# Kernel optimization log

Hardware: AMD Instinct MI355X
Metric: run time of the kernel (lower is better)

The kernel has to match this reference:

```python
import jax, jax.numpy as jnp
import numpy as np

IN_DIM = 256      # in_dim
OUT_DIM = 4608    # out_dim = 6*768 (adaLN projection)
M = 68            # ceil(sqrt(max(in_dim, out_dim)))
PAD = M * M       # 4624 padded (perfect-square) dim
B = 16384         # token batch
INIT_SCALE = 0.02


def setup_inputs() -> dict:
    key = jax.random.key(0)
    k1, k2, k3 = jax.random.split(key, 3)
    x = jax.random.normal(k1, (B, IN_DIM), dtype=jnp.float32)
    # Monarch block-diagonal factors: M blocks of M x M each, scaled per init_scale
    L = jax.random.normal(k2, (M, M, M), dtype=jnp.float32) * INIT_SCALE
    R = jax.random.normal(k3, (M, M, M), dtype=jnp.float32) * INIT_SCALE
    bias = jnp.zeros((OUT_DIM,), dtype=jnp.float32)
    return {"x": x, "L": L, "R": R, "bias": bias}


def _monarch_linear(x, L, R, bias):
    # zero-pad input up to the perfect-square dim n = M*M
    b = x.shape[0]
    xp = jnp.pad(x, ((0, 0), (0, PAD - IN_DIM)))          # [B, PAD]
    x2 = xp.reshape(b, M, M)                               # [B, k=M, p=M]
    # first block-diagonal matmul: per-block x @ L[k]^T
    t1 = jnp.einsum('bkp,kqp->bkq', x2, L)                 # [B, k, q]
    # Monarch inner permutation (block transpose)
    t1 = jnp.swapaxes(t1, 1, 2)                            # [B, l=q, r=k]
    # second block-diagonal matmul
    t2 = jnp.einsum('blr,lsr->bls', t1, R)                 # [B, l, s]
    y = jnp.swapaxes(t2, 1, 2).reshape(b, PAD)             # [B, PAD] (s-major)
    # slice to out_dim, add bias
    return y[:, :OUT_DIM] + bias


def reference(x, L, R, bias):
    return _monarch_linear(x, L, R, bias)
```

## Files before the change

kernel.cpp:

```cpp
#include <hip/hip_runtime.h>


typedef float f4 __attribute__((ext_vector_type(4)));

namespace {
constexpr int MM    = 68;
constexpr int IN_D  = 256;
constexpr int OUT_D = 4608;
constexpr int TT    = 16;
constexpr int NTH   = 256;
constexpr int NJ    = 5;
constexpr int XROW  = IN_D + 4;
constexpr int TPAD  = 4 * MM + 4;
}

template <int P4M>
__device__ __forceinline__ void phaseA(const float* __restrict__ xls,
                                       const float* __restrict__ Lrow0,
                                       float* __restrict__ t1w)
{
  float acc[17];
#pragma unroll
  for (int li = 0; li < 17; ++li) acc[li] = 0.f;

#pragma unroll 1
  for (int p4 = 0; p4 < P4M; ++p4) {
    f4 xv = *(const f4*)(xls + 4 * p4);
    f4 Lv[17];
#pragma unroll
    for (int li = 0; li < 17; ++li)
      Lv[li] = *(const f4*)(Lrow0 + (size_t)li * MM + 4 * p4);
#pragma unroll
    for (int li = 0; li < 17; ++li) {
      acc[li] = fmaf(xv.x, Lv[li].x, acc[li]);
      acc[li] = fmaf(xv.y, Lv[li].y, acc[li]);
      acc[li] = fmaf(xv.z, Lv[li].z, acc[li]);
      acc[li] = fmaf(xv.w, Lv[li].w, acc[li]);
    }
  }
#pragma unroll
  for (int li = 0; li < 17; ++li) t1w[li] = acc[li];
}

__global__ __launch_bounds__(NTH, 4)
void monarch_fused(const float* __restrict__ x, const float* __restrict__ L,
                   const float* __restrict__ R, const float* __restrict__ bias,
                   float* __restrict__ out)
{
  __shared__ float xs[TT * XROW];
  __shared__ float t1s[TT * TPAD];
  const int tid = threadIdx.x;
  const long tb = (long)blockIdx.x * TT;

#pragma unroll
  for (int k = 0; k < (TT * IN_D / 4) / NTH; ++k) {
    int i   = k * NTH + tid;
    int tok = i >> 6;
    int pos = i & 63;
    *(f4*)(&xs[tok * XROW + 4 * pos]) = *(const f4*)(x + (tb + tok) * IN_D + 4 * pos);
  }
  __syncthreads();

  {
    const int tok = tid & 15;
    const int seg = tid >> 4;
    const int r   = seg >> 2;
    const int lq  = seg & 3;
    const float* xls   = &xs[tok * XROW + r * MM];
    const float* Lrow0 = L + (size_t)(r * MM + lq * 17) * MM;
    float*       t1w   = &t1s[tok * TPAD + r * MM + lq * 17];
    if (r < 3) phaseA<17>(xls, Lrow0, t1w);
    else       phaseA<13>(xls, Lrow0, t1w);
  }
  __syncthreads();

  {
    const int g  = tid / 17;
    const int m  = tid - g * 17;
    const int l4 = 4 * m;

#pragma unroll 1
    for (int j = 0; j < NJ; ++j) {
      const int s = g + 15 * j;
      const bool act = (tid < 255) && (s < MM) && (s < MM - 1 || m < 13);
      const int scol = s * MM + l4;
      f4 R0, R1, R2, R3, bv;
      if (act) {
        R0 = *(const f4*)(R + (size_t)(l4 + 0) * (MM * MM) + (size_t)s * MM);
        R1 = *(const f4*)(R + (size_t)(l4 + 1) * (MM * MM) + (size_t)s * MM);
        R2 = *(const f4*)(R + (size_t)(l4 + 2) * (MM * MM) + (size_t)s * MM);
        R3 = *(const f4*)(R + (size_t)(l4 + 3) * (MM * MM) + (size_t)s * MM);
        bv = *(const f4*)(bias + scol);
      }
#pragma unroll 2
      for (int t = 0; t < TT; ++t) {
        if (act) {
          const float* t1p = t1s + t * TPAD + l4;
          f4 a0 = *(const f4*)(t1p);
          f4 a1 = *(const f4*)(t1p + MM);
          f4 a2 = *(const f4*)(t1p + 2 * MM);
          f4 a3 = *(const f4*)(t1p + 3 * MM);
          f4 o;
          o.x = fmaf(a3.x, R0.w, fmaf(a2.x, R0.z, fmaf(a1.x, R0.y, fmaf(a0.x, R0.x, bv.x))));
          o.y = fmaf(a3.y, R1.w, fmaf(a2.y, R1.z, fmaf(a1.y, R1.y, fmaf(a0.y, R1.x, bv.y))));
          o.z = fmaf(a3.z, R2.w, fmaf(a2.z, R2.z, fmaf(a1.z, R2.y, fmaf(a0.z, R2.x, bv.z))));
          o.w = fmaf(a3.w, R3.w, fmaf(a2.w, R3.z, fmaf(a1.w, R3.y, fmaf(a0.w, R3.x, bv.w))));
          *(f4*)(out + (tb + t) * OUT_D + scol) = o;
        }
      }
    }
  }
}

extern "C" void kernel_launch(void* const* d_in, const int* in_sizes, int n_in,
                              void* d_out, int out_size, void* d_ws, size_t ws_size,
                              hipStream_t stream) {
  const float* x    = (const float*)d_in[0];
  const float* L    = (const float*)d_in[1];
  const float* R    = (const float*)d_in[2];
  const float* bias = (const float*)d_in[3];
  float* out = (float*)d_out;

  const int ntok = in_sizes[0] / IN_D;
  monarch_fused<<<ntok / TT, NTH, 0, stream>>>(x, L, R, bias, out);
}
```

Baseline: 91.34 us.

## Interleave first-stage chunks with second-stage output writes inside each block

Phase A now runs in chunks of 4 tokens, with the threads split across token, block and row-quarter. Each chunk's first-stage products are computed while the second stage writes outputs for the previous chunk, with a barrier between chunks. The aim is to overlap the L-side compute with the large output store stream instead of running them as two separate phases. In exchange, R and bias are reloaded once per chunk, there are extra __syncthreads barriers, and the per-thread dot products are shorter.

```diff
diff --git a/kernel.cpp b/kernel.cpp
--- a/kernel.cpp
+++ b/kernel.cpp
@@ -8,30 +8,31 @@
 constexpr int IN_D  = 256;
 constexpr int OUT_D = 4608;
 constexpr int TT    = 16;
+constexpr int QT    = 4;
 constexpr int NTH   = 256;
 constexpr int NJ    = 5;
 constexpr int XROW  = IN_D + 4;
 constexpr int TPAD  = 4 * MM + 4;
 }
 
-template <int P4M>
-__device__ __forceinline__ void phaseA(const float* __restrict__ xls,
-                                       const float* __restrict__ Lrow0,
-                                       float* __restrict__ t1w)
+template <int NLI>
+__device__ __forceinline__ void dotA(const float* __restrict__ xls,
+                                     const float* __restrict__ Lrow0,
+                                     float* __restrict__ t1w, int p4m)
 {
-  float acc[17];
+  float acc[NLI];
 #pragma unroll
-  for (int li = 0; li < 17; ++li) acc[li] = 0.f;
+  for (int li = 0; li < NLI; ++li) acc[li] = 0.f;
 
 #pragma unroll 1
-  for (int p4 = 0; p4 < P4M; ++p4) {
+  for (int p4 = 0; p4 < p4m; ++p4) {
     f4 xv = *(const f4*)(xls + 4 * p4);
-    f4 Lv[17];
+    f4 Lv[NLI];
 #pragma unroll
-    for (int li = 0; li < 17; ++li)
+    for (int li = 0; li < NLI; ++li)
       Lv[li] = *(const f4*)(Lrow0 + (size_t)li * MM + 4 * p4);
 #pragma unroll
-    for (int li = 0; li < 17; ++li) {
+    for (int li = 0; li < NLI; ++li) {
       acc[li] = fmaf(xv.x, Lv[li].x, acc[li]);
       acc[li] = fmaf(xv.y, Lv[li].y, acc[li]);
       acc[li] = fmaf(xv.z, Lv[li].z, acc[li]);
@@ -39,13 +40,13 @@
     }
   }
 #pragma unroll
-  for (int li = 0; li < 17; ++li) t1w[li] = acc[li];
+  for (int li = 0; li < NLI; ++li) t1w[li] = acc[li];
 }
 
 __global__ __launch_bounds__(NTH, 4)
-void monarch_fused(const float* __restrict__ x, const float* __restrict__ L,
-                   const float* __restrict__ R, const float* __restrict__ bias,
-                   float* __restrict__ out)
+void monarch_pipe(const float* __restrict__ x, const float* __restrict__ L,
+                  const float* __restrict__ R, const float* __restrict__ bias,
+                  float* __restrict__ out)
 {
   __shared__ float xs[TT * XROW];
   __shared__ float t1s[TT * TPAD];
@@ -59,26 +60,30 @@
     int pos = i & 63;
     *(f4*)(&xs[tok * XROW + 4 * pos]) = *(const f4*)(x + (tb + tok) * IN_D + 4 * pos);
   }
+
+  const int atok = tid & 3;
+  const int acb  = (tid >> 2) & 15;
+  const int ar   = acb >> 2;
+  const int alq  = acb & 3;
+  const int liq  = tid >> 6;
+  const int li0  = (liq == 0) ? 0 : (4 * liq + 1);
+  const int ap4m = (ar == 3) ? 13 : 17;
+  const float* axls = &xs[atok * XROW + ar * MM];
+  const float* aL0  = L + (size_t)(ar * MM + alq * 17 + li0) * MM;
+  float*       at1w = &t1s[atok * TPAD + ar * MM + alq * 17 + li0];
+
+  const int g  = tid / 17;
+  const int m  = tid - g * 17;
+  const int l4 = 4 * m;
+
   __syncthreads();
 
-  {
-    const int tok = tid & 15;
-    const int seg = tid >> 4;
-    const int r   = seg >> 2;
-    const int lq  = seg & 3;
-    const float* xls   = &xs[tok * XROW + r * MM];
-    const float* Lrow0 = L + (size_t)(r * MM + lq * 17) * MM;
-    float*       t1w   = &t1s[tok * TPAD + r * MM + lq * 17];
-    if (r < 3) phaseA<17>(xls, Lrow0, t1w);
-    else       phaseA<13>(xls, Lrow0, t1w);
-  }
+  if (liq == 0) dotA<5>(axls, aL0, at1w, ap4m);
+  else          dotA<4>(axls, aL0, at1w, ap4m);
   __syncthreads();
 
-  {
-    const int g  = tid / 17;
-    const int m  = tid - g * 17;
-    const int l4 = 4 * m;
-
+#pragma unroll 1
+  for (int q = 0; q < TT / QT; ++q) {
 #pragma unroll 1
     for (int j = 0; j < NJ; ++j) {
       const int s = g + 15 * j;
@@ -92,8 +97,9 @@
         R3 = *(const f4*)(R + (size_t)(l4 + 3) * (MM * MM) + (size_t)s * MM);
         bv = *(const f4*)(bias + scol);
       }
-#pragma unroll 2
-      for (int t = 0; t < TT; ++t) {
+#pragma unroll
+      for (int ti = 0; ti < QT; ++ti) {
+        const int t = q * QT + ti;
         if (act) {
           const float* t1p = t1s + t * TPAD + l4;
           f4 a0 = *(const f4*)(t1p);
@@ -109,6 +115,13 @@
         }
       }
     }
+    if (q < TT / QT - 1) {
+      const float* xq = axls + (q + 1) * QT * XROW;
+      float*       tq = at1w + (q + 1) * QT * TPAD;
+      if (liq == 0) dotA<5>(xq, aL0, tq, ap4m);
+      else          dotA<4>(xq, aL0, tq, ap4m);
+      __syncthreads();
+    }
   }
 }
 
@@ -122,5 +135,5 @@
   float* out = (float*)d_out;
 
   const int ntok = in_sizes[0] / IN_D;
-  monarch_fused<<<ntok / TT, NTH, 0, stream>>>(x, L, R, bias, out);
+  monarch_pipe<<<ntok / TT, NTH, 0, stream>>>(x, L, R, bias, out);
 }
```

Measured after the change: 152.8 us. 1.67x slower.

## Split phase-A reduction across lane quarters with wave shuffle combine

Applied to the files above, without the earlier changes.

Phase A (x times L blocks) is re-partitioned so each wave handles all four input blocks in turn. Its 64 lanes split into 16 tokens by 4 interleaved slices of the p dimension, and partial sums are combined with cross-lane xor shuffles. Previously each thread walked the whole p range for one block. The aim is to cut serial loop length, spread L loads across lanes, and avoid the r==3 divergence inside a wave. In exchange it adds shuffle overhead, redundant tail loads on lanes with q!=0, and an outer loop over r.

```diff
diff --git a/kernel.cpp b/kernel.cpp
--- a/kernel.cpp
+++ b/kernel.cpp
@@ -14,32 +14,49 @@
 constexpr int TPAD  = 4 * MM + 4;
 }
 
-template <int P4M>
-__device__ __forceinline__ void phaseA(const float* __restrict__ xls,
-                                       const float* __restrict__ Lrow0,
-                                       float* __restrict__ t1w)
+template <int FS>
+__device__ __forceinline__ void aPass(const float* __restrict__ xrow,
+                                      const float* __restrict__ Lbase,
+                                      float* __restrict__ t1w, int q)
 {
+  f4 xvr[FS];
+#pragma unroll
+  for (int s = 0; s < FS; ++s)
+    xvr[s] = *(const f4*)(xrow + 4 * (4 * s + q));
+  f4 xvt = *(const f4*)(xrow + 4 * (4 * FS));
+  if (q != 0) xvt = f4{0.f, 0.f, 0.f, 0.f};
+
   float acc[17];
 #pragma unroll
   for (int li = 0; li < 17; ++li) acc[li] = 0.f;
 
-#pragma unroll 1
-  for (int p4 = 0; p4 < P4M; ++p4) {
-    f4 xv = *(const f4*)(xls + 4 * p4);
-    f4 Lv[17];
+#pragma unroll 2
+  for (int li = 0; li < 17; ++li) {
+    const float* Lrow = Lbase + (size_t)li * MM;
+    float a = acc[li];
 #pragma unroll
-    for (int li = 0; li < 17; ++li)
-      Lv[li] = *(const f4*)(Lrow0 + (size_t)li * MM + 4 * p4);
+    for (int s = 0; s < FS; ++s) {
+      f4 Lv = *(const f4*)(Lrow + 4 * (4 * s + q));
+      a = fmaf(xvr[s].x, Lv.x, a);
+      a = fmaf(xvr[s].y, Lv.y, a);
+      a = fmaf(xvr[s].z, Lv.z, a);
+      a = fmaf(xvr[s].w, Lv.w, a);
+    }
+    f4 Lvt = *(const f4*)(Lrow + 4 * (4 * FS));
+    a = fmaf(xvt.x, Lvt.x, a);
+    a = fmaf(xvt.y, Lvt.y, a);
+    a = fmaf(xvt.z, Lvt.z, a);
+    a = fmaf(xvt.w, Lvt.w, a);
+    acc[li] = a;
+  }
+
 #pragma unroll
-    for (int li = 0; li < 17; ++li) {
-      acc[li] = fmaf(xv.x, Lv[li].x, acc[li]);
-      acc[li] = fmaf(xv.y, Lv[li].y, acc[li]);
-      acc[li] = fmaf(xv.z, Lv[li].z, acc[li]);
-      acc[li] = fmaf(xv.w, Lv[li].w, acc[li]);
-    }
+  for (int li = 0; li < 17; ++li) {
+    float v = acc[li];
+    v += __shfl_xor(v, 16, 64);
+    v += __shfl_xor(v, 32, 64);
+    if (q == 0) t1w[li] = v;
   }
-#pragma unroll
-  for (int li = 0; li < 17; ++li) t1w[li] = acc[li];
 }
 
 __global__ __launch_bounds__(NTH, 4)
@@ -62,15 +79,19 @@
   __syncthreads();
 
   {
-    const int tok = tid & 15;
-    const int seg = tid >> 4;
-    const int r   = seg >> 2;
-    const int lq  = seg & 3;
-    const float* xls   = &xs[tok * XROW + r * MM];
-    const float* Lrow0 = L + (size_t)(r * MM + lq * 17) * MM;
-    float*       t1w   = &t1s[tok * TPAD + r * MM + lq * 17];
-    if (r < 3) phaseA<17>(xls, Lrow0, t1w);
-    else       phaseA<13>(xls, Lrow0, t1w);
+    const int lane = tid & 63;
+    const int tok  = lane & 15;
+    const int q    = lane >> 4;
+    const int lq   = tid >> 6;
+
+#pragma unroll 1
+    for (int r = 0; r < 4; ++r) {
+      const float* xrow  = &xs[tok * XROW + r * MM];
+      const float* Lbase = L + (size_t)(r * MM + lq * 17) * MM;
+      float*       t1w   = &t1s[tok * TPAD + r * MM + lq * 17];
+      if (r < 3) aPass<4>(xrow, Lbase, t1w, q);
+      else       aPass<3>(xrow, Lbase, t1w, q);
+    }
   }
   __syncthreads();
 
```

Measured after the change: 101.0 us. +10.5%, slower.

## Collapse Monarch factors into dense bf16 weight and use MFMA GEMM

Applied to the files above, without the earlier changes.

Adds a pre-pass kernel that multiplies the L and R factors into one dense 4608x256 weight matrix (only the 256 live input columns) and stores it in bf16 in the workspace. A second kernel then runs a bf16 MFMA GEMM with double-buffered LDS weight tiles and the x fragments held in registers. This replaces the scalar-FMA two-stage Monarch path with tensor-core work, at the cost of bf16 rounding of x and W (precision loss against the fp32 reference) and an extra packing launch on each call. The old fused kernel is kept as a fallback when the workspace is too small.

```diff
diff --git a/kernel.cpp b/kernel.cpp
--- a/kernel.cpp
+++ b/kernel.cpp
@@ -2,110 +2,220 @@
 
 
 typedef float f4 __attribute__((ext_vector_type(4)));
+typedef short s8v __attribute__((ext_vector_type(8)));
 
 namespace {
 constexpr int MM    = 68;
 constexpr int IN_D  = 256;
 constexpr int OUT_D = 4608;
-constexpr int TT    = 16;
+constexpr int BM    = 64;
 constexpr int NTH   = 256;
-constexpr int NJ    = 5;
-constexpr int XROW  = IN_D + 4;
-constexpr int TPAD  = 4 * MM + 4;
-}
-
+constexpr int PJ    = 128;
+constexpr int WROW  = 264;
+constexpr int NP    = OUT_D / PJ;
+}
+
+__device__ __forceinline__ unsigned short f2bf(float f) {
+  unsigned int u = __float_as_uint(f);
+  u += 0x7FFFu + ((u >> 16) & 1u);
+  return (unsigned short)(u >> 16);
+}
+
+__global__ __launch_bounds__(NTH, 1)
+void pack_w(const float* __restrict__ L, const float* __restrict__ R,
+            unsigned short* __restrict__ Wb)
+{
+  const int j  = blockIdx.x * 8 + (threadIdx.x >> 5);
+  const int c0 = (threadIdx.x & 31) * 8;
+  const int s  = j / MM;
+  const int l  = j - s * MM;
+  unsigned int h[4];
+#pragma unroll
+  for (int i2 = 0; i2 < 4; ++i2) {
+    unsigned int lo, hi;
+#pragma unroll
+    for (int k = 0; k < 2; ++k) {
+      int c = c0 + i2 * 2 + k;
+      int r = c / MM, p = c - r * MM;
+      float w = L[(r * MM + l) * MM + p] * R[(l * MM + s) * MM + r];
+      if (k == 0) lo = f2bf(w); else hi = f2bf(w);
+    }
+    h[i2] = lo | (hi << 16);
+  }
+  uint4 v; v.x = h[0]; v.y = h[1]; v.z = h[2]; v.w = h[3];
+  *(uint4*)(Wb + (size_t)j * IN_D + c0) = v;
+}
+
+__global__ __launch_bounds__(NTH)
+void mono_gemm(const float* __restrict__ x, const unsigned short* __restrict__ Wb,
+               const float* __restrict__ bias, float* __restrict__ out)
+{
+  __shared__ unsigned short wsm[2][PJ][WROW];
+  const int tid  = threadIdx.x;
+  const int lane = tid & 63;
+  const int wv   = tid >> 6;
+  const int lrow = lane & 15;
+  const int lgrp = lane >> 4;
+  const long tb  = (long)blockIdx.x * BM;
+
+  uint4 stg[16];
+  {
+    const unsigned short* src = Wb;
+#pragma unroll
+    for (int k = 0; k < 16; ++k) {
+      int idx = k * NTH + tid;
+      stg[k] = *(const uint4*)(src + (idx >> 5) * IN_D + (idx & 31) * 8);
+    }
+#pragma unroll
+    for (int k = 0; k < 16; ++k) {
+      int idx = k * NTH + tid;
+      *(uint4*)(&wsm[0][idx >> 5][(idx & 31) * 8]) = stg[k];
+    }
+  }
+
+  s8v afr[4][8];
+#pragma unroll
+  for (int mt = 0; mt < 4; ++mt) {
+#pragma unroll
+    for (int ks = 0; ks < 8; ++ks) {
+      const float* xp = x + (tb + mt * 16 + lrow) * IN_D + ks * 32 + lgrp * 8;
+      f4 a = *(const f4*)(xp);
+      f4 b = *(const f4*)(xp + 4);
+      s8v t;
+      t[0] = (short)f2bf(a.x); t[1] = (short)f2bf(a.y);
+      t[2] = (short)f2bf(a.z); t[3] = (short)f2bf(a.w);
+      t[4] = (short)f2bf(b.x); t[5] = (short)f2bf(b.y);
+      t[6] = (short)f2bf(b.z); t[7] = (short)f2bf(b.w);
+      afr[mt][ks] = t;
+    }
+  }
+
+#pragma unroll 1
+  for (int p = 0; p < NP; ++p) {
+    __syncthreads();
+    if (p + 1 < NP) {
+      const unsigned short* src = Wb + (size_t)(p + 1) * PJ * IN_D;
+#pragma unroll
+      for (int k = 0; k < 16; ++k) {
+        int idx = k * NTH + tid;
+        stg[k] = *(const uint4*)(src + (idx >> 5) * IN_D + (idx & 31) * 8);
+      }
+    }
+
+    const unsigned short* buf = &wsm[p & 1][0][0];
+#pragma unroll
+    for (int cj = 0; cj < 2; ++cj) {
+      const int jloc = wv * 32 + cj * 16;
+      const int jg   = p * PJ + jloc + lrow;
+      f4 acc0 = {0.f,0.f,0.f,0.f}, acc1 = {0.f,0.f,0.f,0.f};
+      f4 acc2 = {0.f,0.f,0.f,0.f}, acc3 = {0.f,0.f,0.f,0.f};
+#pragma unroll
+      for (int ks = 0; ks < 8; ++ks) {
+        s8v bf = *(const s8v*)(buf + (jloc + lrow) * WROW + ks * 32 + lgrp * 8);
+        acc0 = __builtin_amdgcn_mfma_f32_16x16x32_bf16(afr[0][ks], bf, acc0, 0, 0, 0);
+        acc1 = __builtin_amdgcn_mfma_f32_16x16x32_bf16(afr[1][ks], bf, acc1, 0, 0, 0);
+        acc2 = __builtin_amdgcn_mfma_f32_16x16x32_bf16(afr[2][ks], bf, acc2, 0, 0, 0);
+        acc3 = __builtin_amdgcn_mfma_f32_16x16x32_bf16(afr[3][ks], bf, acc3, 0, 0, 0);
+      }
+      const float bv = bias[jg];
+      float* ob = out + tb * OUT_D + jg;
+#pragma unroll
+      for (int q = 0; q < 4; ++q) {
+        ob[(size_t)(0 * 16 + lgrp * 4 + q) * OUT_D] = acc0[q] + bv;
+        ob[(size_t)(1 * 16 + lgrp * 4 + q) * OUT_D] = acc1[q] + bv;
+        ob[(size_t)(2 * 16 + lgrp * 4 + q) * OUT_D] = acc2[q] + bv;
+        ob[(size_t)(3 * 16 + lgrp * 4 + q) * OUT_D] = acc3[q] + bv;
+      }
+    }
+
+    if (p + 1 < NP) {
+#pragma unroll
+      for (int k = 0; k < 16; ++k) {
+        int idx = k * NTH + tid;
+        *(uint4*)(&wsm[(p + 1) & 1][idx >> 5][(idx & 31) * 8]) = stg[k];
+      }
+    }
+  }
+}
+
+typedef float f4f __attribute__((ext_vector_type(4)));
+namespace {
+constexpr int TTF  = 16;
+constexpr int XROW = IN_D + 4;
+constexpr int TPAD = 4 * MM + 4;
+}
 template <int P4M>
-__device__ __forceinline__ void phaseA(const float* __restrict__ xls,
-                                       const float* __restrict__ Lrow0,
-                                       float* __restrict__ t1w)
+__device__ __forceinline__ void phaseA_f(const float* xls, const float* Lrow0, float* t1w)
 {
   float acc[17];
 #pragma unroll
   for (int li = 0; li < 17; ++li) acc[li] = 0.f;
-
 #pragma unroll 1
   for (int p4 = 0; p4 < P4M; ++p4) {
-    f4 xv = *(const f4*)(xls + 4 * p4);
-    f4 Lv[17];
-#pragma unroll
-    for (int li = 0; li < 17; ++li)
-      Lv[li] = *(const f4*)(Lrow0 + (size_t)li * MM + 4 * p4);
+    f4f xv = *(const f4f*)(xls + 4 * p4);
+    f4f Lv[17];
+#pragma unroll
+    for (int li = 0; li < 17; ++li) Lv[li] = *(const f4f*)(Lrow0 + (size_t)li * MM + 4 * p4);
 #pragma unroll
     for (int li = 0; li < 17; ++li) {
-      acc[li] = fmaf(xv.x, Lv[li].x, acc[li]);
-      acc[li] = fmaf(xv.y, Lv[li].y, acc[li]);
-      acc[li] = fmaf(xv.z, Lv[li].z, acc[li]);
-      acc[li] = fmaf(xv.w, Lv[li].w, acc[li]);
+      acc[li] = fmaf(xv.x, Lv[li].x, acc[li]); acc[li] = fmaf(xv.y, Lv[li].y, acc[li]);
+      acc[li] = fmaf(xv.z, Lv[li].z, acc[li]); acc[li] = fmaf(xv.w, Lv[li].w, acc[li]);
     }
   }
 #pragma unroll
   for (int li = 0; li < 17; ++li) t1w[li] = acc[li];
 }
-
 __global__ __launch_bounds__(NTH, 4)
 void monarch_fused(const float* __restrict__ x, const float* __restrict__ L,
                    const float* __restrict__ R, const float* __restrict__ bias,
                    float* __restrict__ out)
 {
-  __shared__ float xs[TT * XROW];
-  __shared__ float t1s[TT * TPAD];
+  __shared__ float xs[TTF * XROW];
+  __shared__ float t1s[TTF * TPAD];
   const int tid = threadIdx.x;
-  const long tb = (long)blockIdx.x * TT;
-
-#pragma unroll
-  for (int k = 0; k < (TT * IN_D / 4) / NTH; ++k) {
-    int i   = k * NTH + tid;
-    int tok = i >> 6;
-    int pos = i & 63;
-    *(f4*)(&xs[tok * XROW + 4 * pos]) = *(const f4*)(x + (tb + tok) * IN_D + 4 * pos);
+  const long tb = (long)blockIdx.x * TTF;
+#pragma unroll
+  for (int k = 0; k < (TTF * IN_D / 4) / NTH; ++k) {
+    int i = k * NTH + tid; int tok = i >> 6; int pos = i & 63;
+    *(f4f*)(&xs[tok * XROW + 4 * pos]) = *(const f4f*)(x + (tb + tok) * IN_D + 4 * pos);
   }
   __syncthreads();
-
   {
-    const int tok = tid & 15;
-    const int seg = tid >> 4;
-    const int r   = seg >> 2;
-    const int lq  = seg & 3;
-    const float* xls   = &xs[tok * XROW + r * MM];
+    const int tok = tid & 15; const int seg = tid >> 4;
+    const int r = seg >> 2; const int lq = seg & 3;
+    const float* xls = &xs[tok * XROW + r * MM];
     const float* Lrow0 = L + (size_t)(r * MM + lq * 17) * MM;
-    float*       t1w   = &t1s[tok * TPAD + r * MM + lq * 17];
-    if (r < 3) phaseA<17>(xls, Lrow0, t1w);
-    else       phaseA<13>(xls, Lrow0, t1w);
+    float* t1w = &t1s[tok * TPAD + r * MM + lq * 17];
+    if (r < 3) phaseA_f<17>(xls, Lrow0, t1w); else phaseA_f<13>(xls, Lrow0, t1w);
   }
   __syncthreads();
-
   {
-    const int g  = tid / 17;
-    const int m  = tid - g * 17;
-    const int l4 = 4 * m;
-
+    const int g = tid / 17; const int m = tid - g * 17; const int l4 = 4 * m;
 #pragma unroll 1
-    for (int j = 0; j < NJ; ++j) {
+    for (int j = 0; j < 5; ++j) {
       const int s = g + 15 * j;
       const bool act = (tid < 255) && (s < MM) && (s < MM - 1 || m < 13);
       const int scol = s * MM + l4;
-      f4 R0, R1, R2, R3, bv;
+      f4f R0, R1, R2, R3, bv;
       if (act) {
-        R0 = *(const f4*)(R + (size_t)(l4 + 0) * (MM * MM) + (size_t)s * MM);
-        R1 = *(const f4*)(R + (size_t)(l4 + 1) * (MM * MM) + (size_t)s * MM);
-        R2 = *(const f4*)(R + (size_t)(l4 + 2) * (MM * MM) + (size_t)s * MM);
-        R3 = *(const f4*)(R + (size_t)(l4 + 3) * (MM * MM) + (size_t)s * MM);
-        bv = *(const f4*)(bias + scol);
+        R0 = *(const f4f*)(R + (size_t)(l4 + 0) * (MM * MM) + (size_t)s * MM);
+        R1 = *(const f4f*)(R + (size_t)(l4 + 1) * (MM * MM) + (size_t)s * MM);
+        R2 = *(const f4f*)(R + (size_t)(l4 + 2) * (MM * MM) + (size_t)s * MM);
+        R3 = *(const f4f*)(R + (size_t)(l4 + 3) * (MM * MM) + (size_t)s * MM);
+        bv = *(const f4f*)(bias + scol);
       }
 #pragma unroll 2
-      for (int t = 0; t < TT; ++t) {
+      for (int t = 0; t < TTF; ++t) {
         if (act) {
           const float* t1p = t1s + t * TPAD + l4;
-          f4 a0 = *(const f4*)(t1p);
-          f4 a1 = *(const f4*)(t1p + MM);
-          f4 a2 = *(const f4*)(t1p + 2 * MM);
-          f4 a3 = *(const f4*)(t1p + 3 * MM);
-          f4 o;
+          f4f a0 = *(const f4f*)(t1p); f4f a1 = *(const f4f*)(t1p + MM);
+          f4f a2 = *(const f4f*)(t1p + 2 * MM); f4f a3 = *(const f4f*)(t1p + 3 * MM);
+          f4f o;
           o.x = fmaf(a3.x, R0.w, fmaf(a2.x, R0.z, fmaf(a1.x, R0.y, fmaf(a0.x, R0.x, bv.x))));
           o.y = fmaf(a3.y, R1.w, fmaf(a2.y, R1.z, fmaf(a1.y, R1.y, fmaf(a0.y, R1.x, bv.y))));
           o.z = fmaf(a3.z, R2.w, fmaf(a2.z, R2.z, fmaf(a1.z, R2.y, fmaf(a0.z, R2.x, bv.z))));
           o.w = fmaf(a3.w, R3.w, fmaf(a2.w, R3.z, fmaf(a1.w, R3.y, fmaf(a0.w, R3.x, bv.w))));
-          *(f4*)(out + (tb + t) * OUT_D + scol) = o;
+          *(f4f*)(out + (tb + t) * OUT_D + scol) = o;
         }
       }
     }
@@ -122,5 +232,13 @@
   float* out = (float*)d_out;
 
   const int ntok = in_sizes[0] / IN_D;
-  monarch_fused<<<ntok / TT, NTH, 0, stream>>>(x, L, R, bias, out);
-}
+  const size_t wb_bytes = (size_t)OUT_D * IN_D * sizeof(unsigned short);
+
+  if (ws_size >= wb_bytes) {
+    unsigned short* Wb = (unsigned short*)d_ws;
+    pack_w<<<OUT_D / 8, NTH, 0, stream>>>(L, R, Wb);
+    mono_gemm<<<ntok / BM, NTH, 0, stream>>>(x, Wb, bias, out);
+  } else {
+    monarch_fused<<<ntok / TTF, NTH, 0, stream>>>(x, L, R, bias, out);
+  }
+}
```

New measurement: 216.4 us. +136.9%, slower.
